# Kernel optimization log

Hardware: AMD Instinct MI355X
Metric: run time of the kernel (lower is better)

Reference implementation:

```python
import jax, jax.numpy as jnp
import numpy as np

B, L, D, H, DK, DV, FF, V, N = 1, 1024, 1024, 16, 64, 64, 4096, 32000, 12


def _ln(x, s, b):
    mu = jnp.mean(x, axis=-1, keepdims=True)
    var = jnp.mean((x - mu) ** 2, axis=-1, keepdims=True)
    return (x - mu) / jnp.sqrt(var + 1e-5) * s + b


def _pe(length, d):
    # interleaved sin/cos positional encoding, matching stack([sin,cos],-1).view(L,D)
    i = 2.0 * jnp.arange(d // 2, dtype=jnp.float32)
    base = 10000.0 ** (-i / d)
    half = jnp.arange(length, dtype=jnp.float32)[:, None] * base[None, :]  # [L, D/2]
    return jnp.stack([jnp.sin(half), jnp.cos(half)], axis=-1).reshape(length, d)


def setup_inputs() -> dict:
    key = jax.random.key(0)
    ks = jax.random.split(key, 8)
    s = 0.02
    return {
        "tokens": jax.random.randint(ks[0], (B, L), 0, V),
        "emb": jax.random.normal(ks[1], (V, D), jnp.float32) * s,
        "final_b": jnp.zeros((V,), jnp.float32),
        "Wq": jax.random.normal(ks[2], (N, H, D, DK), jnp.float32) * s,
        "Wk": jax.random.normal(ks[3], (N, H, D, DK), jnp.float32) * s,
        "Wv": jax.random.normal(ks[4], (N, H, D, DV), jnp.float32) * s,
        "Wo": jax.random.normal(ks[5], (N, H * DV, D), jnp.float32) * s,
        "ln1_s": jnp.ones((N, D), jnp.float32),
        "ln1_b": jnp.zeros((N, D), jnp.float32),
        "W1": jax.random.normal(ks[6], (N, D, FF), jnp.float32) * s,
        "b1": jnp.zeros((N, FF), jnp.float32),
        "W2": jax.random.normal(ks[7], (N, FF, D), jnp.float32) * s,
        "b2": jnp.zeros((N, D), jnp.float32),
        "ln2_s": jnp.ones((N, D), jnp.float32),
        "ln2_b": jnp.zeros((N, D), jnp.float32),
    }


def _forward(tokens, emb, final_b, Wq, Wk, Wv, Wo, ln1_s, ln1_b, W1, b1, W2, b2, ln2_s, ln2_b):
    a = emb[tokens] * jnp.sqrt(jnp.float32(3.0 * D))  # tied-weight scaling
    a = a + (a + _pe(L, D))  # faithful to `a += pe(a)` where pe returns x + PE
    mask = jnp.tril(jnp.ones((L, L), dtype=bool))
    scale = 1.0 / jnp.sqrt(jnp.float32(D))  # original divides by sqrt(d_model), not d_k

    def layer(x, p):
        wq, wk, wv, wo, s1, sb1, w1, bb1, w2, bb2, s2, sb2 = p
        q = jnp.einsum('bld,hdk->bhlk', x, wq)
        k = jnp.einsum('bld,hdk->bhlk', x, wk)
        v = jnp.einsum('bld,hdv->bhlv', x, wv)
        scores = jnp.einsum('bhqk,bhmk->bhqm', q, k) * scale  # [B,H,L,L]
        scores = jnp.where(mask, scores, -jnp.inf)  # causal triu(-inf)
        attn = jax.nn.softmax(scores, axis=-1)
        o = jnp.einsum('bhqm,bhmv->bhqv', attn, v)
        o = o.transpose(0, 2, 1, 3).reshape(x.shape[0], L, H * DV)  # concat heads
        x = _ln(x + o @ wo, s1, sb1)  # post-LN residual
        f = jax.nn.relu(x @ w1 + bb1) @ w2 + bb2
        x = _ln(x + f, s2, sb2)
        return x, None

    x, _ = jax.lax.scan(layer, a, (Wq, Wk, Wv, Wo, ln1_s, ln1_b, W1, b1, W2, b2, ln2_s, ln2_b))
    return x @ emb.T + final_b  # tied output projection with bias


def reference(tokens, emb, final_b, Wq, Wk, Wv, Wo, ln1_s, ln1_b, W1, b1, W2, b2, ln2_s, ln2_b):
    return _forward(tokens, emb, final_b, Wq, Wk, Wv, Wo, ln1_s, ln1_b, W1, b1, W2, b2, ln2_s, ln2_b)
```

## Files before the change

kernel.cpp:

```cpp
#include <hip/hip_runtime.h>

typedef unsigned short u16;
typedef __attribute__((ext_vector_type(8))) short short8;
typedef __attribute__((ext_vector_type(4))) float f32x4;
typedef __attribute__((ext_vector_type(4))) u16 u16x4;

#define LSEQ   1024
#define DMODEL 1024
#define NHEAD  16
#define DHEAD  64
#define DFF    4096
#define NLAYER 12
#define NVOCAB 32000

__device__ __forceinline__ u16 f2b(float f) {
  union { float f; unsigned u; } x; x.f = f;
  unsigned r = x.u + 0x7fffu + ((x.u >> 16) & 1u);
  return (u16)(r >> 16);
}
__device__ __forceinline__ float b2f(u16 u) {
  union { unsigned u; float f; } x; x.u = ((unsigned)u) << 16; return x.f;
}

__device__ __forceinline__ f32x4 mfma16(short8 a, short8 b, f32x4 c) {
  return __builtin_amdgcn_mfma_f32_16x16x32_bf16(a, b, c, 0, 0, 0);
}

__device__ __forceinline__ void gload16(const u16* g, u16* l) {
  __builtin_amdgcn_global_load_lds(
      (const __attribute__((address_space(1))) void*)g,
      (__attribute__((address_space(3))) void*)l, 16, 0, 0);
}

template<int N> __device__ __forceinline__ void waitvm() {
  if constexpr (N <= 0)      asm volatile("s_waitcnt vmcnt(0)" ::: "memory");
  else if constexpr (N == 1) asm volatile("s_waitcnt vmcnt(1)" ::: "memory");
  else if constexpr (N == 2) asm volatile("s_waitcnt vmcnt(2)" ::: "memory");
  else if constexpr (N == 3) asm volatile("s_waitcnt vmcnt(3)" ::: "memory");
  else if constexpr (N == 4) asm volatile("s_waitcnt vmcnt(4)" ::: "memory");
  else if constexpr (N == 5) asm volatile("s_waitcnt vmcnt(5)" ::: "memory");
  else if constexpr (N == 6) asm volatile("s_waitcnt vmcnt(6)" ::: "memory");
  else                       asm volatile("s_waitcnt vmcnt(8)" ::: "memory");
}

__global__ __launch_bounds__(256) void embed_k(const int* __restrict__ tok,
    const float* __restrict__ emb, float* __restrict__ x, u16* __restrict__ xb)
{
  const int l = blockIdx.x;
  const int d0 = threadIdx.x * 4;
  const int t = tok[l];
  const float lf = (float)l;
  float o[4]; u16 obv[4];
#pragma unroll
  for (int j = 0; j < 4; ++j) {
    int d = d0 + j;
    int p = d >> 1;
    float ang = lf * powf(10000.0f, -(float)(2 * p) / 1024.0f);
    float pe = (d & 1) ? cosf(ang) : sinf(ang);
    float val = 2.0f * emb[(size_t)t * DMODEL + d] * 55.42562584220407f + pe;
    o[j] = val; obv[j] = f2b(val);
  }
  *reinterpret_cast<float4*>(x + (size_t)l * DMODEL + d0) = make_float4(o[0], o[1], o[2], o[3]);
  u16x4 vb = { obv[0], obv[1], obv[2], obv[3] };
  *reinterpret_cast<u16x4*>(xb + (size_t)l * DMODEL + d0) = vb;
}

__global__ __launch_bounds__(256) void ln_k(const float* __restrict__ xin,
    const float* __restrict__ ypart, int P, const float* __restrict__ ybias,
    const float* __restrict__ s, const float* __restrict__ b,
    float* __restrict__ xout, u16* __restrict__ xbout)
{
  const int row = blockIdx.x, tid = threadIdx.x;
  const int d0 = tid * 4;
  float4 xv = *reinterpret_cast<const float4*>(xin + (size_t)row * DMODEL + d0);
  float t0 = xv.x, t1 = xv.y, t2 = xv.z, t3 = xv.w;
#pragma unroll 2
  for (int p = 0; p < P; ++p) {
    float4 yv = *reinterpret_cast<const float4*>(ypart + (size_t)p * (LSEQ * DMODEL) + (size_t)row * DMODEL + d0);
    t0 += yv.x; t1 += yv.y; t2 += yv.z; t3 += yv.w;
  }
  if (ybias) {
    float4 bb = *reinterpret_cast<const float4*>(ybias + d0);
    t0 += bb.x; t1 += bb.y; t2 += bb.z; t3 += bb.w;
  }
  float sum = t0 + t1 + t2 + t3;
  float sq  = t0 * t0 + t1 * t1 + t2 * t2 + t3 * t3;
#pragma unroll
  for (int d = 1; d < 64; d <<= 1) { sum += __shfl_xor(sum, d); sq += __shfl_xor(sq, d); }
  __shared__ float ssum[4], ssq[4];
  const int wid = tid >> 6;
  if ((tid & 63) == 0) { ssum[wid] = sum; ssq[wid] = sq; }
  __syncthreads();
  sum = ssum[0] + ssum[1] + ssum[2] + ssum[3];
  sq  = ssq[0] + ssq[1] + ssq[2] + ssq[3];
  const float mu = sum * (1.0f / 1024.0f);
  const float var = sq * (1.0f / 1024.0f) - mu * mu;
  const float rstd = rsqrtf(var + 1e-5f);
  float4 sv = *reinterpret_cast<const float4*>(s + d0);
  float4 bv = *reinterpret_cast<const float4*>(b + d0);
  float o0 = (t0 - mu) * rstd * sv.x + bv.x;
  float o1 = (t1 - mu) * rstd * sv.y + bv.y;
  float o2 = (t2 - mu) * rstd * sv.z + bv.z;
  float o3 = (t3 - mu) * rstd * sv.w + bv.w;
  *reinterpret_cast<float4*>(xout + (size_t)row * DMODEL + d0) = make_float4(o0, o1, o2, o3);
  u16x4 vb = { f2b(o0), f2b(o1), f2b(o2), f2b(o3) };
  *reinterpret_cast<u16x4*>(xbout + (size_t)row * DMODEL + d0) = vb;
}

__global__ __launch_bounds__(256) void qkvred_k(const u16* __restrict__ sp,
    u16* __restrict__ q, u16* __restrict__ k, u16* __restrict__ v)
{
  const size_t idx = ((size_t)blockIdx.x * 256 + threadIdx.x) * 8;
  const int row = (int)(idx / 3072), c0 = (int)(idx % 3072);
  short8 a = *reinterpret_cast<const short8*>(sp + idx);
  short8 b = *reinterpret_cast<const short8*>(sp + (size_t)LSEQ * 3072 + idx);
  const int sel = c0 >> 10;
  const float sc = (sel == 0) ? 0.03125f : 1.0f;
  short8 o;
#pragma unroll
  for (int j = 0; j < 8; ++j)
    o[j] = (short)f2b((b2f((u16)a[j]) + b2f((u16)b[j])) * sc);
  u16* dst = (sel == 0 ? q : (sel == 1 ? k : v)) + (size_t)row * DMODEL + (c0 & 1023);
  *reinterpret_cast<short8*>(dst) = o;
}

__global__ __launch_bounds__(256) void ffred_k(const u16* __restrict__ sp,
    const float* __restrict__ bias, u16* __restrict__ out)
{
  const size_t idx = ((size_t)blockIdx.x * 256 + threadIdx.x) * 8;
  const int c0 = (int)(idx % DFF);
  short8 a = *reinterpret_cast<const short8*>(sp + idx);
  short8 b = *reinterpret_cast<const short8*>(sp + (size_t)LSEQ * DFF + idx);
  short8 o;
#pragma unroll
  for (int j = 0; j < 8; ++j) {
    float val = b2f((u16)a[j]) + b2f((u16)b[j]) + bias[c0 + j];
    o[j] = (short)f2b(fmaxf(val, 0.0f));
  }
  *reinterpret_cast<short8*>(out + idx) = o;
}

__global__ __launch_bounds__(256) void tconv_k(const float* __restrict__ in, u16* __restrict__ out,
                                               int R, int C, int zper, int lstride, int obase, int zstride)
{
  __shared__ float t[64][65];
  const int rt = blockIdx.y * 64, ct = blockIdx.x * 64;
  const int z = blockIdx.z;
  in += (size_t)z * zstride;
  const int tr = threadIdx.x >> 4, tc = threadIdx.x & 15;
#pragma unroll
  for (int i = 0; i < 4; ++i) {
    int r = i * 16 + tr;
    float4 v = *reinterpret_cast<const float4*>(in + (size_t)(rt + r) * C + ct + tc * 4);
    t[r][tc * 4 + 0] = v.x; t[r][tc * 4 + 1] = v.y;
    t[r][tc * 4 + 2] = v.z; t[r][tc * 4 + 3] = v.w;
  }
  __syncthreads();
  const size_t orow0 = (size_t)(z / zper) * lstride + (size_t)(z % zper) * C + obase + ct;
#pragma unroll
  for (int i = 0; i < 4; ++i) {
    int c = i * 16 + tr;
    u16x4 o;
    o[0] = f2b(t[tc * 4 + 0][c]); o[1] = f2b(t[tc * 4 + 1][c]);
    o[2] = f2b(t[tc * 4 + 2][c]); o[3] = f2b(t[tc * 4 + 3][c]);
    *reinterpret_cast<u16x4*>(out + (orow0 + c) * R + rt + tc * 4) = o;
  }
}

__global__ __launch_bounds__(256) void ec_k(const float* __restrict__ in, u16* __restrict__ out)
{
  const size_t i = ((size_t)blockIdx.x * 256 + threadIdx.x) * 8;
  float4 a = *reinterpret_cast<const float4*>(in + i);
  float4 b = *reinterpret_cast<const float4*>(in + i + 4);
  short8 o;
  o[0] = f2b(a.x); o[1] = f2b(a.y); o[2] = f2b(a.z); o[3] = f2b(a.w);
  o[4] = f2b(b.x); o[5] = f2b(b.y); o[6] = f2b(b.z); o[7] = f2b(b.w);
  *reinterpret_cast<short8*>(out + i) = o;
}

template<int BM, int BN, int BK, int BSRC, bool BIAS, bool RELU, int OUTMODE, int KSPLIT>
__global__ __launch_bounds__(256) void gemm_bt(
    const u16* __restrict__ A, int lda,
    const void* __restrict__ Bp, int ldb,
    const float* __restrict__ bias,
    void* __restrict__ Cv, int ldc, int Ktot)
{
  constexpr int CPR = BK / 8;
  constexpr int SWM = CPR - 1;
  constexpr int LA = (BM * CPR) / 256;
  constexpr int LB = (BN * CPR) / 256;
  constexpr int LT = LA + LB;
  __shared__ u16 As[3][BM * BK];
  __shared__ u16 Bs[3][BN * BK];
  const int tid = threadIdx.x, lane = tid & 63, wid = tid >> 6;
  const int nwg = gridDim.x * gridDim.y;
  const int flat = blockIdx.y * gridDim.x + blockIdx.x;
  const int qq = nwg >> 3;
  const int ni = (flat & 7) * qq + (flat >> 3);
  const int m0 = (ni % gridDim.x) * BM, n0 = (ni / gridDim.x) * BN;
  const int kbase = (KSPLIT > 1) ? blockIdx.z * (Ktot / KSPLIT) : 0;
  const int klen  = (KSPLIT > 1) ? (Ktot / KSPLIT) : Ktot;
  constexpr int FM = BM / 32, FN = BN / 32;
  constexpr int KS = BK / 32;
  const int wm = (wid >> 1) * (BM / 2), wn = (wid & 1) * (BN / 2);
  f32x4 acc[FM][FN] = {};

  if constexpr (BSRC == 0) {
    const u16* Bt = (const u16*)Bp;
    auto stage = [&](int slot, int k0) {
#pragma unroll
      for (int i = 0; i < LA; ++i) {
        int c = i * 256 + tid;
        int row = c / CPR, p0 = c % CPR;
        int part = p0 ^ (((row * CPR) >> 3) & SWM);
        gload16(A + (size_t)(m0 + row) * lda + k0 + part * 8,
                &As[slot][(i * 256 + wid * 64) * 8]);
      }
#pragma unroll
      for (int i = 0; i < LB; ++i) {
        int c = i * 256 + tid;
        int row = c / CPR, p0 = c % CPR;
        int part = p0 ^ (((row * CPR) >> 3) & SWM);
        gload16(Bt + (size_t)(n0 + row) * ldb + k0 + part * 8,
                &Bs[slot][(i * 256 + wid * 64) * 8]);
      }
    };

    const int NT = klen / BK;
    stage(0, kbase);
    stage(1, kbase + BK);
    waitvm<LT>();
    __builtin_amdgcn_s_barrier();
    asm volatile("" ::: "memory");

    int cur = 0, stg = 2;
    for (int t = 0; t < NT; ++t) {
      const bool more = (t + 2 < NT);
      if (more) stage(stg, kbase + (t + 2) * BK);
      asm volatile("" ::: "memory");
      short8 a[KS][FM], b[KS][FN];
#pragma unroll
      for (int ks = 0; ks < KS; ++ks) {
#pragma unroll
        for (int fm = 0; fm < FM; ++fm) {
          int row = wm + fm * 16 + (lane & 15);
          int pidx = (ks * 4 + (lane >> 4)) ^ (((row * CPR) >> 3) & SWM);
          a[ks][fm] = *reinterpret_cast<const short8*>(&As[cur][row * BK + pidx * 8]);
        }
#pragma unroll
        for (int fn = 0; fn < FN; ++fn) {
          int row = wn + fn * 16 + (lane & 15);
          int pidx = (ks * 4 + (lane >> 4)) ^ (((row * CPR) >> 3) & SWM);
          b[ks][fn] = *reinterpret_cast<const short8*>(&Bs[cur][row * BK + pidx * 8]);
        }
      }
#pragma unroll
      for (int ks = 0; ks < KS; ++ks)
#pragma unroll
        for (int fm = 0; fm < FM; ++fm)
#pragma unroll
          for (int fn = 0; fn < FN; ++fn)
            acc[fm][fn] = mfma16(a[ks][fm], b[ks][fn], acc[fm][fn]);
      if (more) waitvm<LT>(); else waitvm<0>();
      __builtin_amdgcn_s_barrier();
      asm volatile("" ::: "memory");
      cur = (cur == 2) ? 0 : cur + 1;
      stg = (stg == 2) ? 0 : stg + 1;
    }
  } else {
    const float* Bf = (const float*)Bp;
    for (int k0 = 0; k0 < Ktot; k0 += BK) {
#pragma unroll
      for (int i = 0; i < LA; ++i) {
        int c = i * 256 + tid;
        int row = c / CPR, part = c % CPR;
        gload16(A + (size_t)(m0 + row) * lda + k0 + part * 8,
                &As[0][(i * 256 + wid * 64) * 8]);
      }
      {
        int row = tid >> 1, kh = (tid & 1) * 16;
        const float* src = Bf + (size_t)(n0 + row) * ldb + k0 + kh;
        float4 v0 = *reinterpret_cast<const float4*>(src);
        float4 v1 = *reinterpret_cast<const float4*>(src + 4);
        float4 v2 = *reinterpret_cast<const float4*>(src + 8);
        float4 v3 = *reinterpret_cast<const float4*>(src + 12);
        short8 p0, p1;
        p0[0] = f2b(v0.x); p0[1] = f2b(v0.y); p0[2] = f2b(v0.z); p0[3] = f2b(v0.w);
        p0[4] = f2b(v1.x); p0[5] = f2b(v1.y); p0[6] = f2b(v1.z); p0[7] = f2b(v1.w);
        p1[0] = f2b(v2.x); p1[1] = f2b(v2.y); p1[2] = f2b(v2.z); p1[3] = f2b(v2.w);
        p1[4] = f2b(v3.x); p1[5] = f2b(v3.y); p1[6] = f2b(v3.z); p1[7] = f2b(v3.w);
        *reinterpret_cast<short8*>(&Bs[0][row * BK + kh])     = p0;
        *reinterpret_cast<short8*>(&Bs[0][row * BK + kh + 8]) = p1;
      }
      __syncthreads();
      short8 a[KS][FM], b[KS][FN];
#pragma unroll
      for (int ks = 0; ks < KS; ++ks) {
#pragma unroll
        for (int fm = 0; fm < FM; ++fm) {
          int row = wm + fm * 16 + (lane & 15);
          a[ks][fm] = *reinterpret_cast<const short8*>(&As[0][row * BK + (ks * 4 + (lane >> 4)) * 8]);
        }
#pragma unroll
        for (int fn = 0; fn < FN; ++fn) {
          int row = wn + fn * 16 + (lane & 15);
          b[ks][fn] = *reinterpret_cast<const short8*>(&Bs[0][row * BK + (ks * 4 + (lane >> 4)) * 8]);
        }
      }
#pragma unroll
      for (int ks = 0; ks < KS; ++ks)
#pragma unroll
        for (int fm = 0; fm < FM; ++fm)
#pragma unroll
          for (int fn = 0; fn < FN; ++fn)
            acc[fm][fn] = mfma16(a[ks][fm], b[ks][fn], acc[fm][fn]);
      __syncthreads();
    }
  }

  const size_t pbase = (KSPLIT > 1) ? (size_t)blockIdx.z * gridDim.x * BM * ldc : 0;
#pragma unroll
  for (int fm = 0; fm < FM; ++fm) {
#pragma unroll
    for (int fn = 0; fn < FN; ++fn) {
#pragma unroll
      for (int r = 0; r < 4; ++r) {
        int row = m0 + wm + fm * 16 + (lane >> 4) * 4 + r;
        int col = n0 + wn + fn * 16 + (lane & 15);
        float val = acc[fm][fn][r];
        if (BIAS) val += bias[col];
        if (RELU) val = fmaxf(val, 0.0f);
        if (OUTMODE == 0) {
          ((float*)Cv)[pbase + (size_t)row * ldc + col] = val;
        } else if (OUTMODE == 1) {
          ((u16*)Cv)[(size_t)row * ldc + col] = f2b(val);
        } else if (OUTMODE == 3) {
          ((u16*)Cv)[pbase + (size_t)row * ldc + col] = f2b(val);
        } else {
          int sel = col >> 10, cc = col & 1023;
          if (sel == 0) val *= 0.03125f;
          ((u16*)Cv)[(size_t)sel * (LSEQ * DMODEL) + (size_t)row * DMODEL + cc] = f2b(val);
        }
      }
    }
  }
}

__global__ __launch_bounds__(256) void attn_k(const u16* __restrict__ q,
    const u16* __restrict__ kmat, const u16* __restrict__ v, u16* __restrict__ o)
{
  __shared__ u16 Ks[64][72];
  __shared__ u16 Vt[64][72];
  __shared__ u16 Pl[4][16][72];
  const int tid = threadIdx.x, lane = tid & 63, wid = tid >> 6;
  const int h = blockIdx.y, qt = blockIdx.x;
  const int qw0 = qt * 64 + wid * 16;
  const int qrow = qw0 + (lane & 15);
  const short8 aq0 = *reinterpret_cast<const short8*>(q + (size_t)qrow * DMODEL + h * DHEAD + (lane >> 4) * 8);
  const short8 aq1 = *reinterpret_cast<const short8*>(q + (size_t)qrow * DMODEL + h * DHEAD + 32 + (lane >> 4) * 8);
  float m_run[4], l_run[4];
  f32x4 oacc[4] = {};
#pragma unroll
  for (int r = 0; r < 4; ++r) { m_run[r] = -1e30f; l_run[r] = 0.0f; }
  const int kvend = qt * 64 + 64;

  const int kvi = tid >> 2, c16 = (tid & 3) * 16;
  short8 kr0, kr1, vr0, vr1;
  auto loadregs = [&](int kv0) {
    const u16* kp = kmat + (size_t)(kv0 + kvi) * DMODEL + h * DHEAD + c16;
    kr0 = *reinterpret_cast<const short8*>(kp);
    kr1 = *reinterpret_cast<const short8*>(kp + 8);
    const u16* vp = v + (size_t)(kv0 + kvi) * DMODEL + h * DHEAD + c16;
    vr0 = *reinterpret_cast<const short8*>(vp);
    vr1 = *reinterpret_cast<const short8*>(vp + 8);
  };
  loadregs(0);

  for (int kv0 = 0; kv0 < kvend; kv0 += 64) {
    __syncthreads();
    *reinterpret_cast<short8*>(&Ks[kvi][c16])     = kr0;
    *reinterpret_cast<short8*>(&Ks[kvi][c16 + 8]) = kr1;
#pragma unroll
    for (int j = 0; j < 8; ++j) { Vt[c16 + j][kvi] = (u16)vr0[j]; Vt[c16 + 8 + j][kvi] = (u16)vr1[j]; }
    __syncthreads();
    if (kv0 + 64 < kvend) loadregs(kv0 + 64);

    float sm[4][4];
#pragma unroll
    for (int t2 = 0; t2 < 4; ++t2) {
      short8 bk0 = *reinterpret_cast<const short8*>(&Ks[t2 * 16 + (lane & 15)][(lane >> 4) * 8]);
      short8 bk1 = *reinterpret_cast<const short8*>(&Ks[t2 * 16 + (lane & 15)][32 + (lane >> 4) * 8]);
      f32x4 s4 = {};
      s4 = mfma16(aq0, bk0, s4);
      s4 = mfma16(aq1, bk1, s4);
#pragma unroll
      for (int r = 0; r < 4; ++r) {
        int rowg = qw0 + (lane >> 4) * 4 + r;
        int colg = kv0 + t2 * 16 + (lane & 15);
        sm[t2][r] = (colg <= rowg) ? s4[r] : -1e30f;
      }
    }
    float alpha[4], p[4][4];
#pragma unroll
    for (int r = 0; r < 4; ++r) {
      float mx = fmaxf(fmaxf(sm[0][r], sm[1][r]), fmaxf(sm[2][r], sm[3][r]));
#pragma unroll
      for (int d = 1; d < 16; d <<= 1) mx = fmaxf(mx, __shfl_xor(mx, d));
      float mn = fmaxf(m_run[r], mx);
      alpha[r] = __expf(m_run[r] - mn);
      float ps = 0.0f;
#pragma unroll
      for (int t2 = 0; t2 < 4; ++t2) { p[t2][r] = __expf(sm[t2][r] - mn); ps += p[t2][r]; }
#pragma unroll
      for (int d = 1; d < 16; d <<= 1) ps += __shfl_xor(ps, d);
      l_run[r] = l_run[r] * alpha[r] + ps;
      m_run[r] = mn;
    }
#pragma unroll
    for (int fn = 0; fn < 4; ++fn) {
      f32x4 t = oacc[fn];
      t[0] *= alpha[0]; t[1] *= alpha[1]; t[2] *= alpha[2]; t[3] *= alpha[3];
      oacc[fn] = t;
    }
#pragma unroll
    for (int r = 0; r < 4; ++r) {
      int rit = (lane >> 4) * 4 + r;
#pragma unroll
      for (int t2 = 0; t2 < 4; ++t2)
        Pl[wid][rit][t2 * 16 + (lane & 15)] = f2b(p[t2][r]);
    }
    short8 pa0 = *reinterpret_cast<const short8*>(&Pl[wid][lane & 15][(lane >> 4) * 8]);
    short8 pa1 = *reinterpret_cast<const short8*>(&Pl[wid][lane & 15][32 + (lane >> 4) * 8]);
#pragma unroll
    for (int fn = 0; fn < 4; ++fn) {
      short8 bv0 = *reinterpret_cast<const short8*>(&Vt[fn * 16 + (lane & 15)][(lane >> 4) * 8]);
      short8 bv1 = *reinterpret_cast<const short8*>(&Vt[fn * 16 + (lane & 15)][32 + (lane >> 4) * 8]);
      oacc[fn] = mfma16(pa0, bv0, oacc[fn]);
      oacc[fn] = mfma16(pa1, bv1, oacc[fn]);
    }
  }
#pragma unroll
  for (int fn = 0; fn < 4; ++fn) {
#pragma unroll
    for (int r = 0; r < 4; ++r) {
      int row = qw0 + (lane >> 4) * 4 + r;
      float val = oacc[fn][r] / l_run[r];
      o[(size_t)row * DMODEL + h * DHEAD + fn * 16 + (lane & 15)] = f2b(val);
    }
  }
}

extern "C" void kernel_launch(void* const* d_in, const int* in_sizes, int n_in,
                              void* d_out, int out_size, void* d_ws, size_t ws_size,
                              hipStream_t stream) {
  (void)in_sizes; (void)n_in; (void)out_size;
  const int*   tok    = (const int*)d_in[0];
  const float* emb    = (const float*)d_in[1];
  const float* finalb = (const float*)d_in[2];
  const float* Wq     = (const float*)d_in[3];
  const float* Wk     = (const float*)d_in[4];
  const float* Wv     = (const float*)d_in[5];
  const float* Wo     = (const float*)d_in[6];
  const float* ln1s   = (const float*)d_in[7];
  const float* ln1b   = (const float*)d_in[8];
  const float* W1     = (const float*)d_in[9];
  const float* b1     = (const float*)d_in[10];
  const float* W2     = (const float*)d_in[11];
  const float* b2     = (const float*)d_in[12];
  const float* ln2s   = (const float*)d_in[13];
  const float* ln2b   = (const float*)d_in[14];
  float* out = (float*)d_out;

  float* x   = (float*)d_ws;
  float* y   = x + LSEQ * DMODEL;
  u16* xb    = (u16*)(y + LSEQ * DMODEL);
  u16* qb    = xb + LSEQ * DMODEL;
  u16* kb    = qb + LSEQ * DMODEL;
  u16* vb    = kb + LSEQ * DMODEL;
  u16* ob    = vb + LSEQ * DMODEL;
  u16* h1    = ob + LSEQ * DMODEL;
  u16* wbase = h1 + LSEQ * DFF;
  float* woPart  = (float*)h1;
  float* ff2Part = (float*)qb;

  const size_t eQKV = (size_t)3 * DMODEL * DMODEL;
  const size_t eWO  = (size_t)DMODEL * DMODEL;
  const size_t eW1  = (size_t)DFF * DMODEL;
  const size_t eW2  = (size_t)DMODEL * DFF;
  const size_t perL = eQKV + eWO + eW1 + eW2;
  const size_t eEMB = (size_t)NVOCAB * DMODEL;
  const size_t eSP  = (size_t)2 * LSEQ * DFF;
  const size_t actE = (size_t)(wbase - (u16*)d_ws);
  const size_t bigNeed = (actE + NLAYER * perL + eEMB + eSP) * 2;
  const size_t midNeed = (actE + perL + eEMB) * 2;
  const int mode = ws_size >= bigNeed ? 2 : (ws_size >= midNeed ? 1 : 0);
  const int WL = (mode == 2) ? NLAYER : 1;

  u16* qkvT = wbase;
  u16* woT  = qkvT + WL * eQKV;
  u16* w1T  = woT  + WL * eWO;
  u16* w2T  = w1T  + WL * eW1;
  u16* embT = w2T  + WL * eW2;
  u16* sp   = embT + eEMB;

  if (mode == 2) {
    tconv_k<<<dim3(1, 16, 192), 256, 0, stream>>>(Wq, qkvT, DMODEL, DHEAD, 16, 3 * DMODEL, 0,    DMODEL * DHEAD);
    tconv_k<<<dim3(1, 16, 192), 256, 0, stream>>>(Wk, qkvT, DMODEL, DHEAD, 16, 3 * DMODEL, 1024, DMODEL * DHEAD);
    tconv_k<<<dim3(1, 16, 192), 256, 0, stream>>>(Wv, qkvT, DMODEL, DHEAD, 16, 3 * DMODEL, 2048, DMODEL * DHEAD);
    tconv_k<<<dim3(16, 16, 12), 256, 0, stream>>>(Wo, woT, DMODEL, DMODEL, 1, DMODEL, 0, DMODEL * DMODEL);
    tconv_k<<<dim3(64, 16, 12), 256, 0, stream>>>(W1, w1T, DMODEL, DFF, 1, DFF, 0, DMODEL * DFF);
    tconv_k<<<dim3(16, 64, 12), 256, 0, stream>>>(W2, w2T, DFF, DMODEL, 1, DMODEL, 0, DFF * DMODEL);
    ec_k<<<(NVOCAB * DMODEL) / 2048, 256, 0, stream>>>(emb, embT);
  } else if (mode == 1) {
    ec_k<<<(NVOCAB * DMODEL) / 2048, 256, 0, stream>>>(emb, embT);
  }

  embed_k<<<LSEQ, 256, 0, stream>>>(tok, emb, x, xb);

  for (int l = 0; l < NLAYER; ++l) {
    const float* wq  = Wq + (size_t)l * NHEAD * DMODEL * DHEAD;
    const float* wk  = Wk + (size_t)l * NHEAD * DMODEL * DHEAD;
    const float* wv  = Wv + (size_t)l * NHEAD * DMODEL * DHEAD;
    const float* wo  = Wo + (size_t)l * DMODEL * DMODEL;
    const float* w1  = W1 + (size_t)l * DMODEL * DFF;
    const float* b1l = b1 + (size_t)l * DFF;
    const float* w2  = W2 + (size_t)l * DFF * DMODEL;
    const float* b2l = b2 + (size_t)l * DMODEL;
    u16* qkvTl = qkvT + (mode == 2 ? (size_t)l * eQKV : 0);
    u16* woTl  = woT  + (mode == 2 ? (size_t)l * eWO  : 0);
    u16* w1Tl  = w1T  + (mode == 2 ? (size_t)l * eW1  : 0);
    u16* w2Tl  = w2T  + (mode == 2 ? (size_t)l * eW2  : 0);

    if (mode < 2) {
      tconv_k<<<dim3(1, 16, 16), 256, 0, stream>>>(wq, qkvTl, DMODEL, DHEAD, 16, 0, 0,    DMODEL * DHEAD);
      tconv_k<<<dim3(1, 16, 16), 256, 0, stream>>>(wk, qkvTl, DMODEL, DHEAD, 16, 0, 1024, DMODEL * DHEAD);
      tconv_k<<<dim3(1, 16, 16), 256, 0, stream>>>(wv, qkvTl, DMODEL, DHEAD, 16, 0, 2048, DMODEL * DHEAD);
      tconv_k<<<dim3(16, 16, 1), 256, 0, stream>>>(wo, woTl, DMODEL, DMODEL, 1, 0, 0, 0);
      tconv_k<<<dim3(64, 16, 1), 256, 0, stream>>>(w1, w1Tl, DMODEL, DFF, 1, 0, 0, 0);
      tconv_k<<<dim3(16, 64, 1), 256, 0, stream>>>(w2, w2Tl, DFF, DMODEL, 1, 0, 0, 0);
    }

    if (mode == 2) {
      gemm_bt<128, 128, 32, 0, false, false, 3, 2><<<dim3(8, 24, 2), 256, 0, stream>>>(
          xb, DMODEL, qkvTl, DMODEL, nullptr, sp, 3 * DMODEL, DMODEL);
      qkvred_k<<<(LSEQ * 3 * DMODEL) / 2048, 256, 0, stream>>>(sp, qb, kb, vb);
    } else {
      gemm_bt<64, 64, 64, 0, false, false, 2, 1><<<dim3(16, 48), 256, 0, stream>>>(
          xb, DMODEL, qkvTl, DMODEL, nullptr, qb, DMODEL, DMODEL);
    }
    attn_k<<<dim3(16, 16), 256, 0, stream>>>(qb, kb, vb, ob);
    gemm_bt<64, 64, 64, 0, false, false, 0, 2><<<dim3(16, 16, 2), 256, 0, stream>>>(
        ob, DMODEL, woTl, DMODEL, nullptr, woPart, DMODEL, DMODEL);
    ln_k<<<LSEQ, 256, 0, stream>>>(x, woPart, 2, nullptr,
        ln1s + (size_t)l * DMODEL, ln1b + (size_t)l * DMODEL, x, xb);
    if (mode == 2) {
      gemm_bt<128, 128, 32, 0, false, false, 3, 2><<<dim3(8, 32, 2), 256, 0, stream>>>(
          xb, DMODEL, w1Tl, DMODEL, nullptr, sp, DFF, DMODEL);
      ffred_k<<<(LSEQ * DFF) / 2048, 256, 0, stream>>>(sp, b1l, h1);
    } else {
      gemm_bt<64, 64, 64, 0, true, true, 1, 1><<<dim3(16, 64), 256, 0, stream>>>(
          xb, DMODEL, w1Tl, DMODEL, b1l, h1, DFF, DMODEL);
    }
    gemm_bt<64, 64, 64, 0, false, false, 0, 2><<<dim3(16, 16, 2), 256, 0, stream>>>(
        h1, DFF, w2Tl, DFF, nullptr, ff2Part, DMODEL, DFF);
    ln_k<<<LSEQ, 256, 0, stream>>>(x, ff2Part, 2, b2l,
        ln2s + (size_t)l * DMODEL, ln2b + (size_t)l * DMODEL, x, xb);
  }

  if (mode >= 1) {
    gemm_bt<128, 128, 32, 0, true, false, 0, 1><<<dim3(8, 250), 256, 0, stream>>>(
        xb, DMODEL, embT, DMODEL, finalb, out, NVOCAB, DMODEL);
  } else {
    gemm_bt<128, 128, 32, 1, true, false, 0, 1><<<dim3(8, 250), 256, 0, stream>>>(
        xb, DMODEL, emb, DMODEL, finalb, out, NVOCAB, DMODEL);
  }
}
```

Measured before the change: 1.890 ms.

## Fuse QKV split-K reduction into attention; split-K FF2 into bf16 partials

Removes the separate qkvred kernel by having attention read both bf16 split-K partials of Q, K and V directly, summing and scaling them while loading. The FF2 GEMM in the big-workspace mode now uses 128x128 tiles with an 8-way split-K that writes bf16 partials, and a new LayerNorm variant sums those eight partials. This cuts a launch and an intermediate Q/K/V round trip, and gives FF2 more parallelism. In exchange, attention re-reads and re-reduces K/V partials for every query tile, and partial sums are rounded to bf16 before reduction.

```diff
diff --git a/kernel.cpp b/kernel.cpp
--- a/kernel.cpp
+++ b/kernel.cpp
@@ -107,21 +107,46 @@
   *reinterpret_cast<u16x4*>(xbout + (size_t)row * DMODEL + d0) = vb;
 }
 
-__global__ __launch_bounds__(256) void qkvred_k(const u16* __restrict__ sp,
-    u16* __restrict__ q, u16* __restrict__ k, u16* __restrict__ v)
-{
-  const size_t idx = ((size_t)blockIdx.x * 256 + threadIdx.x) * 8;
-  const int row = (int)(idx / 3072), c0 = (int)(idx % 3072);
-  short8 a = *reinterpret_cast<const short8*>(sp + idx);
-  short8 b = *reinterpret_cast<const short8*>(sp + (size_t)LSEQ * 3072 + idx);
-  const int sel = c0 >> 10;
-  const float sc = (sel == 0) ? 0.03125f : 1.0f;
-  short8 o;
-#pragma unroll
-  for (int j = 0; j < 8; ++j)
-    o[j] = (short)f2b((b2f((u16)a[j]) + b2f((u16)b[j])) * sc);
-  u16* dst = (sel == 0 ? q : (sel == 1 ? k : v)) + (size_t)row * DMODEL + (c0 & 1023);
-  *reinterpret_cast<short8*>(dst) = o;
+__global__ __launch_bounds__(256) void lnb_k(const float* __restrict__ xin,
+    const u16* __restrict__ ypart, int P, const float* __restrict__ ybias,
+    const float* __restrict__ s, const float* __restrict__ b,
+    float* __restrict__ xout, u16* __restrict__ xbout)
+{
+  const int row = blockIdx.x, tid = threadIdx.x;
+  const int d0 = tid * 4;
+  float4 xv = *reinterpret_cast<const float4*>(xin + (size_t)row * DMODEL + d0);
+  float t0 = xv.x, t1 = xv.y, t2 = xv.z, t3 = xv.w;
+#pragma unroll 4
+  for (int p = 0; p < P; ++p) {
+    u16x4 yv = *reinterpret_cast<const u16x4*>(ypart + (size_t)p * (LSEQ * DMODEL) + (size_t)row * DMODEL + d0);
+    t0 += b2f(yv[0]); t1 += b2f(yv[1]); t2 += b2f(yv[2]); t3 += b2f(yv[3]);
+  }
+  if (ybias) {
+    float4 bb = *reinterpret_cast<const float4*>(ybias + d0);
+    t0 += bb.x; t1 += bb.y; t2 += bb.z; t3 += bb.w;
+  }
+  float sum = t0 + t1 + t2 + t3;
+  float sq  = t0 * t0 + t1 * t1 + t2 * t2 + t3 * t3;
+#pragma unroll
+  for (int d = 1; d < 64; d <<= 1) { sum += __shfl_xor(sum, d); sq += __shfl_xor(sq, d); }
+  __shared__ float ssum[4], ssq[4];
+  const int wid = tid >> 6;
+  if ((tid & 63) == 0) { ssum[wid] = sum; ssq[wid] = sq; }
+  __syncthreads();
+  sum = ssum[0] + ssum[1] + ssum[2] + ssum[3];
+  sq  = ssq[0] + ssq[1] + ssq[2] + ssq[3];
+  const float mu = sum * (1.0f / 1024.0f);
+  const float var = sq * (1.0f / 1024.0f) - mu * mu;
+  const float rstd = rsqrtf(var + 1e-5f);
+  float4 sv = *reinterpret_cast<const float4*>(s + d0);
+  float4 bv = *reinterpret_cast<const float4*>(b + d0);
+  float o0 = (t0 - mu) * rstd * sv.x + bv.x;
+  float o1 = (t1 - mu) * rstd * sv.y + bv.y;
+  float o2 = (t2 - mu) * rstd * sv.z + bv.z;
+  float o3 = (t3 - mu) * rstd * sv.w + bv.w;
+  *reinterpret_cast<float4*>(xout + (size_t)row * DMODEL + d0) = make_float4(o0, o1, o2, o3);
+  u16x4 vb = { f2b(o0), f2b(o1), f2b(o2), f2b(o3) };
+  *reinterpret_cast<u16x4*>(xbout + (size_t)row * DMODEL + d0) = vb;
 }
 
 __global__ __launch_bounds__(256) void ffred_k(const u16* __restrict__ sp,
@@ -346,6 +371,7 @@
   }
 }
 
+template<int FUSE>
 __global__ __launch_bounds__(256) void attn_k(const u16* __restrict__ q,
     const u16* __restrict__ kmat, const u16* __restrict__ v, u16* __restrict__ o)
 {
@@ -356,8 +382,23 @@
   const int h = blockIdx.y, qt = blockIdx.x;
   const int qw0 = qt * 64 + wid * 16;
   const int qrow = qw0 + (lane & 15);
-  const short8 aq0 = *reinterpret_cast<const short8*>(q + (size_t)qrow * DMODEL + h * DHEAD + (lane >> 4) * 8);
-  const short8 aq1 = *reinterpret_cast<const short8*>(q + (size_t)qrow * DMODEL + h * DHEAD + 32 + (lane >> 4) * 8);
+  const size_t PLQ = (size_t)LSEQ * 3072;
+  short8 aq0, aq1;
+  if constexpr (FUSE) {
+    const u16* qp = q + (size_t)qrow * 3072 + h * DHEAD + (lane >> 4) * 8;
+    short8 a0 = *reinterpret_cast<const short8*>(qp);
+    short8 b0 = *reinterpret_cast<const short8*>(qp + PLQ);
+    short8 a1 = *reinterpret_cast<const short8*>(qp + 32);
+    short8 b1 = *reinterpret_cast<const short8*>(qp + 32 + PLQ);
+#pragma unroll
+    for (int j = 0; j < 8; ++j) {
+      aq0[j] = (short)f2b((b2f((u16)a0[j]) + b2f((u16)b0[j])) * 0.03125f);
+      aq1[j] = (short)f2b((b2f((u16)a1[j]) + b2f((u16)b1[j])) * 0.03125f);
+    }
+  } else {
+    aq0 = *reinterpret_cast<const short8*>(q + (size_t)qrow * DMODEL + h * DHEAD + (lane >> 4) * 8);
+    aq1 = *reinterpret_cast<const short8*>(q + (size_t)qrow * DMODEL + h * DHEAD + 32 + (lane >> 4) * 8);
+  }
   float m_run[4], l_run[4];
   f32x4 oacc[4] = {};
 #pragma unroll
@@ -366,22 +407,52 @@
 
   const int kvi = tid >> 2, c16 = (tid & 3) * 16;
   short8 kr0, kr1, vr0, vr1;
+  short8 kr0b, kr1b, vr0b, vr1b;
   auto loadregs = [&](int kv0) {
-    const u16* kp = kmat + (size_t)(kv0 + kvi) * DMODEL + h * DHEAD + c16;
-    kr0 = *reinterpret_cast<const short8*>(kp);
-    kr1 = *reinterpret_cast<const short8*>(kp + 8);
-    const u16* vp = v + (size_t)(kv0 + kvi) * DMODEL + h * DHEAD + c16;
-    vr0 = *reinterpret_cast<const short8*>(vp);
-    vr1 = *reinterpret_cast<const short8*>(vp + 8);
+    if constexpr (FUSE) {
+      const u16* kp = q + (size_t)(kv0 + kvi) * 3072 + 1024 + h * DHEAD + c16;
+      kr0  = *reinterpret_cast<const short8*>(kp);
+      kr1  = *reinterpret_cast<const short8*>(kp + 8);
+      kr0b = *reinterpret_cast<const short8*>(kp + PLQ);
+      kr1b = *reinterpret_cast<const short8*>(kp + 8 + PLQ);
+      const u16* vp = q + (size_t)(kv0 + kvi) * 3072 + 2048 + h * DHEAD + c16;
+      vr0  = *reinterpret_cast<const short8*>(vp);
+      vr1  = *reinterpret_cast<const short8*>(vp + 8);
+      vr0b = *reinterpret_cast<const short8*>(vp + PLQ);
+      vr1b = *reinterpret_cast<const short8*>(vp + 8 + PLQ);
+    } else {
+      const u16* kp = kmat + (size_t)(kv0 + kvi) * DMODEL + h * DHEAD + c16;
+      kr0 = *reinterpret_cast<const short8*>(kp);
+      kr1 = *reinterpret_cast<const short8*>(kp + 8);
+      const u16* vp = v + (size_t)(kv0 + kvi) * DMODEL + h * DHEAD + c16;
+      vr0 = *reinterpret_cast<const short8*>(vp);
+      vr1 = *reinterpret_cast<const short8*>(vp + 8);
+    }
   };
   loadregs(0);
 
   for (int kv0 = 0; kv0 < kvend; kv0 += 64) {
     __syncthreads();
-    *reinterpret_cast<short8*>(&Ks[kvi][c16])     = kr0;
-    *reinterpret_cast<short8*>(&Ks[kvi][c16 + 8]) = kr1;
-#pragma unroll
-    for (int j = 0; j < 8; ++j) { Vt[c16 + j][kvi] = (u16)vr0[j]; Vt[c16 + 8 + j][kvi] = (u16)vr1[j]; }
+    if constexpr (FUSE) {
+      short8 ko0, ko1;
+#pragma unroll
+      for (int j = 0; j < 8; ++j) {
+        ko0[j] = (short)f2b(b2f((u16)kr0[j]) + b2f((u16)kr0b[j]));
+        ko1[j] = (short)f2b(b2f((u16)kr1[j]) + b2f((u16)kr1b[j]));
+      }
+      *reinterpret_cast<short8*>(&Ks[kvi][c16])     = ko0;
+      *reinterpret_cast<short8*>(&Ks[kvi][c16 + 8]) = ko1;
+#pragma unroll
+      for (int j = 0; j < 8; ++j) {
+        Vt[c16 + j][kvi]     = f2b(b2f((u16)vr0[j]) + b2f((u16)vr0b[j]));
+        Vt[c16 + 8 + j][kvi] = f2b(b2f((u16)vr1[j]) + b2f((u16)vr1b[j]));
+      }
+    } else {
+      *reinterpret_cast<short8*>(&Ks[kvi][c16])     = kr0;
+      *reinterpret_cast<short8*>(&Ks[kvi][c16 + 8]) = kr1;
+#pragma unroll
+      for (int j = 0; j < 8; ++j) { Vt[c16 + j][kvi] = (u16)vr0[j]; Vt[c16 + 8 + j][kvi] = (u16)vr1[j]; }
+    }
     __syncthreads();
     if (kv0 + 64 < kvend) loadregs(kv0 + 64);
 
@@ -480,8 +551,7 @@
   u16* ob    = vb + LSEQ * DMODEL;
   u16* h1    = ob + LSEQ * DMODEL;
   u16* wbase = h1 + LSEQ * DFF;
-  float* woPart  = (float*)h1;
-  float* ff2Part = (float*)qb;
+  float* woPart = (float*)h1;
 
   const size_t eQKV = (size_t)3 * DMODEL * DMODEL;
   const size_t eWO  = (size_t)DMODEL * DMODEL;
@@ -543,12 +613,12 @@
     if (mode == 2) {
       gemm_bt<128, 128, 32, 0, false, false, 3, 2><<<dim3(8, 24, 2), 256, 0, stream>>>(
           xb, DMODEL, qkvTl, DMODEL, nullptr, sp, 3 * DMODEL, DMODEL);
-      qkvred_k<<<(LSEQ * 3 * DMODEL) / 2048, 256, 0, stream>>>(sp, qb, kb, vb);
+      attn_k<1><<<dim3(16, 16), 256, 0, stream>>>(sp, nullptr, nullptr, ob);
     } else {
       gemm_bt<64, 64, 64, 0, false, false, 2, 1><<<dim3(16, 48), 256, 0, stream>>>(
           xb, DMODEL, qkvTl, DMODEL, nullptr, qb, DMODEL, DMODEL);
-    }
-    attn_k<<<dim3(16, 16), 256, 0, stream>>>(qb, kb, vb, ob);
+      attn_k<0><<<dim3(16, 16), 256, 0, stream>>>(qb, kb, vb, ob);
+    }
     gemm_bt<64, 64, 64, 0, false, false, 0, 2><<<dim3(16, 16, 2), 256, 0, stream>>>(
         ob, DMODEL, woTl, DMODEL, nullptr, woPart, DMODEL, DMODEL);
     ln_k<<<LSEQ, 256, 0, stream>>>(x, woPart, 2, nullptr,
@@ -557,14 +627,18 @@
       gemm_bt<128, 128, 32, 0, false, false, 3, 2><<<dim3(8, 32, 2), 256, 0, stream>>>(
           xb, DMODEL, w1Tl, DMODEL, nullptr, sp, DFF, DMODEL);
       ffred_k<<<(LSEQ * DFF) / 2048, 256, 0, stream>>>(sp, b1l, h1);
+      gemm_bt<128, 128, 32, 0, false, false, 3, 8><<<dim3(8, 8, 8), 256, 0, stream>>>(
+          h1, DFF, w2Tl, DFF, nullptr, sp, DMODEL, DFF);
+      lnb_k<<<LSEQ, 256, 0, stream>>>(x, sp, 8, b2l,
+          ln2s + (size_t)l * DMODEL, ln2b + (size_t)l * DMODEL, x, xb);
     } else {
       gemm_bt<64, 64, 64, 0, true, true, 1, 1><<<dim3(16, 64), 256, 0, stream>>>(
           xb, DMODEL, w1Tl, DMODEL, b1l, h1, DFF, DMODEL);
-    }
-    gemm_bt<64, 64, 64, 0, false, false, 0, 2><<<dim3(16, 16, 2), 256, 0, stream>>>(
-        h1, DFF, w2Tl, DFF, nullptr, ff2Part, DMODEL, DFF);
-    ln_k<<<LSEQ, 256, 0, stream>>>(x, ff2Part, 2, b2l,
-        ln2s + (size_t)l * DMODEL, ln2b + (size_t)l * DMODEL, x, xb);
+      gemm_bt<64, 64, 64, 0, false, false, 0, 2><<<dim3(16, 16, 2), 256, 0, stream>>>(
+          h1, DFF, w2Tl, DFF, nullptr, (float*)qb, DMODEL, DFF);
+      ln_k<<<LSEQ, 256, 0, stream>>>(x, (float*)qb, 2, b2l,
+          ln2s + (size_t)l * DMODEL, ln2b + (size_t)l * DMODEL, x, xb);
+    }
   }
 
   if (mode >= 1) {
```

New measurement: 1.790 ms. 1.06x faster.
